# Kernel optimization log

Hardware: AMD Instinct MI355X
Metric: run time of the kernel (lower is better)

The kernel has to match this reference:

```python
import jax, jax.numpy as jnp
import numpy as np

B, T, S = 4, 2048, 512
HID, ND, NH = 2048, 1024, 16
HD = HID // NH  # 128
GATING_INIT = -4.0


def setup_inputs() -> dict:
    key = jax.random.key(0)
    ks = jax.random.split(key, 12)
    sc_h = 1.0 / np.sqrt(HID)
    sc_n = 1.0 / np.sqrt(ND)
    mask = jax.random.bernoulli(ks[2], 0.9, (B, S))
    mask = mask.at[:, 0].set(True)  # avoid fully-masked rows (NaN softmax)
    return {
        "hidden_states": jax.random.normal(ks[0], (B, T, HID), jnp.float32),
        "notes": jax.random.normal(ks[1], (B, S, ND), jnp.float32),
        "notes_mask": mask,
        "q_w": jax.random.normal(ks[3], (HID, HID), jnp.float32) * sc_h,
        "q_b": jax.random.normal(ks[4], (HID,), jnp.float32) * 0.01,
        "k_w": jax.random.normal(ks[5], (HID, ND), jnp.float32) * sc_n,
        "k_b": jax.random.normal(ks[6], (HID,), jnp.float32) * 0.01,
        "v_w": jax.random.normal(ks[7], (HID, ND), jnp.float32) * sc_n,
        "v_b": jax.random.normal(ks[8], (HID,), jnp.float32) * 0.01,
        "o_w": jax.random.normal(ks[9], (HID, HID), jnp.float32) * sc_h,
        "o_b": jax.random.normal(ks[10], (HID,), jnp.float32) * 0.01,
        "gate": jnp.full((1,), GATING_INIT, jnp.float32),
    }


def reference(hidden_states, notes, notes_mask, q_w, q_b, k_w, k_b, v_w, v_b, o_w, o_b, gate):
    # projections (torch Linear: x @ W^T + b)
    q = hidden_states @ q_w.T + q_b            # (B,T,HID)
    k = notes @ k_w.T + k_b                    # (B,S,HID)
    v = notes @ v_w.T + v_b                    # (B,S,HID)
    q = q.reshape(B, T, NH, HD).transpose(0, 2, 1, 3)  # (B,H,T,D)
    k = k.reshape(B, S, NH, HD).transpose(0, 2, 1, 3)  # (B,H,S,D)
    v = v.reshape(B, S, NH, HD).transpose(0, 2, 1, 3)
    scores = jnp.einsum("bhtd,bhsd->bhts", q, k) / jnp.sqrt(jnp.float32(HD))
    scores = jnp.where(notes_mask[:, None, None, :], scores, -jnp.inf)
    attn = jax.nn.softmax(scores, axis=-1)
    context = jnp.einsum("bhts,bhsd->bhtd", attn, v)   # (B,H,T,D)
    g = jax.nn.sigmoid(gate).reshape(1, 1, 1, 1)
    context = (g * context).transpose(0, 2, 1, 3).reshape(B, T, HID)
    delta = context @ o_w.T + o_b
    return delta
```

## Files before the change

kernel.cpp:

```cpp
#include <hip/hip_runtime.h>
#include <hip/hip_bf16.h>
#include <stdint.h>

#define B_ 4
#define T_ 2048
#define S_ 512
#define HID_ 2048
#define ND_ 1024
#define NH_ 16
#define HD_ 128

typedef unsigned short u16;
typedef unsigned int u32;
typedef __attribute__((ext_vector_type(8))) short bf16x8;
typedef __attribute__((ext_vector_type(4))) float f32x4;
typedef __attribute__((ext_vector_type(16))) float f32x16;
typedef __attribute__((ext_vector_type(4))) float f4;
typedef __attribute__((ext_vector_type(4))) u16 us4;
typedef __attribute__((ext_vector_type(8))) u16 us8;
typedef __attribute__((ext_vector_type(4))) u32 u32x4;

__device__ inline u16 f2bf(float f) {
  unsigned u = __builtin_bit_cast(unsigned, f);
  u += 0x7FFFu + ((u >> 16) & 1u);
  return (u16)(u >> 16);
}

__device__ inline u32 cvtpk(float lo, float hi) {
  u32 r;
  asm("v_cvt_pk_bf16_f32 %0, %1, %2" : "=v"(r) : "v"(lo), "v"(hi));
  return r;
}

__device__ inline f32x4 mfma16(bf16x8 a, bf16x8 b, f32x4 c) {
  return __builtin_amdgcn_mfma_f32_16x16x32_bf16(a, b, c, 0, 0, 0);
}
__device__ inline f32x16 mfma32(bf16x8 a, bf16x8 b, f32x16 c) {
  return __builtin_amdgcn_mfma_f32_32x32x16_bf16(a, b, c, 0, 0, 0);
}

__device__ inline void gload_lds16(const u16* g, u16* l) {
  __builtin_amdgcn_global_load_lds(
      (const __attribute__((address_space(1))) unsigned int*)g,
      (__attribute__((address_space(3))) unsigned int*)l, 16, 0, 0);
}

#define FENCED_BARRIER() asm volatile("s_barrier" ::: "memory")

__global__ __launch_bounds__(256) void convert_all(
    const float* __restrict__ h, const float* __restrict__ n,
    const float* __restrict__ qw, const float* __restrict__ kw,
    const float* __restrict__ vw, const float* __restrict__ ow,
    u16* __restrict__ dh, u16* __restrict__ dn, u16* __restrict__ dqw,
    u16* __restrict__ dkw, u16* __restrict__ dvw, u16* __restrict__ dow) {
  const int C0 = 4194304;
  const int C1 = C0 + 524288;
  const int C2 = C1 + 1048576;
  const int C3 = C2 + 524288;
  const int C4 = C3 + 524288;
  const int C5 = C4 + 1048576;
  for (int c = blockIdx.x * blockDim.x + threadIdx.x; c < C5;
       c += gridDim.x * blockDim.x) {
    const float* s; u16* d; int o;
    if (c < C0)      { s = h;  d = dh;  o = c; }
    else if (c < C1) { s = n;  d = dn;  o = c - C0; }
    else if (c < C2) { s = qw; d = dqw; o = c - C1; }
    else if (c < C3) { s = kw; d = dkw; o = c - C2; }
    else if (c < C4) { s = vw; d = dvw; o = c - C3; }
    else             { s = ow; d = dow; o = c - C4; }
    f4 v = ((const f4*)s)[o];
    us4 r = { f2bf(v[0]), f2bf(v[1]), f2bf(v[2]), f2bf(v[3]) };
    ((us4*)d)[o] = r;
  }
}

template <bool OUT_BF16>
__global__ __launch_bounds__(256) void gemm_bt(
    const u16* __restrict__ A, const u16* __restrict__ Bm,
    const float* __restrict__ bias, void* __restrict__ Cout,
    int M, int N, int K) {
  __shared__ u16 As[128 * 32];
  __shared__ u16 Bs[128 * 32];
  const int tid = threadIdx.x;
  const int lane = tid & 63;
  const int wave = tid >> 6;
  const int wr = (wave >> 1) * 64;
  const int wc = (wave & 1) * 64;
  const int c15 = lane & 15;
  const int g = lane >> 4;
  const int bx = blockIdx.x, by = blockIdx.y;

  const u16* gA = A + (size_t)(by * 128 + (tid >> 2)) * K + (tid & 3) * 8;
  const u16* gB = Bm + (size_t)(bx * 128 + (tid >> 2)) * K + (tid & 3) * 8;

  f32x4 acc[4][4];
#pragma unroll
  for (int i = 0; i < 4; ++i)
#pragma unroll
    for (int j = 0; j < 4; ++j) acc[i][j] = (f32x4){0.f, 0.f, 0.f, 0.f};

  for (int k0 = 0; k0 < K; k0 += 32) {
    gload_lds16(gA + k0, &As[wave * 512]);
    gload_lds16(gA + (size_t)64 * K + k0, &As[2048 + wave * 512]);
    gload_lds16(gB + k0, &Bs[wave * 512]);
    gload_lds16(gB + (size_t)64 * K + k0, &Bs[2048 + wave * 512]);
    __syncthreads();
    bf16x8 af[4], bfr[4];
#pragma unroll
    for (int mt = 0; mt < 4; ++mt)
      af[mt] = *(const bf16x8*)&As[(wr + mt * 16 + c15) * 32 + g * 8];
#pragma unroll
    for (int nt = 0; nt < 4; ++nt)
      bfr[nt] = *(const bf16x8*)&Bs[(wc + nt * 16 + c15) * 32 + g * 8];
#pragma unroll
    for (int mt = 0; mt < 4; ++mt)
#pragma unroll
      for (int nt = 0; nt < 4; ++nt)
        acc[mt][nt] = mfma16(af[mt], bfr[nt], acc[mt][nt]);
    __syncthreads();
  }

#pragma unroll
  for (int mt = 0; mt < 4; ++mt)
#pragma unroll
    for (int nt = 0; nt < 4; ++nt) {
      const int m = by * 128 + wr + mt * 16 + g * 4;
      const int n = bx * 128 + wc + nt * 16 + c15;
      const float bv = bias[n];
#pragma unroll
      for (int r = 0; r < 4; ++r) {
        const float v = acc[mt][nt][r] + bv;
        if (OUT_BF16)
          ((u16*)Cout)[(size_t)(m + r) * N + n] = f2bf(v);
        else
          ((float*)Cout)[(size_t)(m + r) * N + n] = v;
      }
    }
}

template <bool OUT_BF16>
__global__ __launch_bounds__(512, 2) void gemm_pipe(
    const u16* __restrict__ A, const u16* __restrict__ Bm,
    const float* __restrict__ bias, void* __restrict__ Cout,
    int M, int N, int K) {
  extern __shared__ u16 lds[];
  const int tid = threadIdx.x;
  const int lane = tid & 63, wave = tid >> 6;
  const int wm = wave >> 2, wn = wave & 3;
  const int c15 = lane & 15, g = lane >> 4;
  const int bid = blockIdx.y * gridDim.x + blockIdx.x;
  const int sw = (bid & 7) * 32 + (bid >> 3);
  const int bn = sw & 7, bm = sw >> 3;
  const int NT = K >> 5;

  const int srow = tid >> 2;
  const int sx = (tid & 3) ^ ((srow >> 1) & 3);
  const u16* pa0 = A + (size_t)(bm * 256 + srow) * K + sx * 8;
  const u16* pa1 = A + (size_t)(bm * 256 + 128 + srow) * K + sx * 8;
  const u16* pb0 = Bm + (size_t)(bn * 256 + srow) * K + sx * 8;
  const u16* pb1 = Bm + (size_t)(bn * 256 + 128 + srow) * K + sx * 8;

  const int xr = (c15 >> 1) & 3;
  const int aoff = wm * 4096 + c15 * 32 + (g ^ xr) * 8;
  const int boff = 8192 + wn * 2048 + c15 * 32 + (g ^ xr) * 8;

  f32x4 acc[8][4];
#pragma unroll
  for (int i = 0; i < 8; ++i)
#pragma unroll
    for (int j = 0; j < 4; ++j) acc[i][j] = (f32x4){0.f, 0.f, 0.f, 0.f};

  {
    u16* sA = lds + wave * 512;
    u16* sB = lds + 8192 + wave * 512;
    gload_lds16(pa0, sA);          gload_lds16(pa1, sA + 4096);
    gload_lds16(pb0, sB);          gload_lds16(pb1, sB + 4096);
    pa0 += 32; pa1 += 32; pb0 += 32; pb1 += 32;
    gload_lds16(pa0, sA + 16384);  gload_lds16(pa1, sA + 20480);
    gload_lds16(pb0, sB + 16384);  gload_lds16(pb1, sB + 20480);
    pa0 += 32; pa1 += 32; pb0 += 32; pb1 += 32;
  }
  asm volatile("s_waitcnt vmcnt(4)" ::: "memory");
  FENCED_BARRIER();

  for (int t = 0; t < NT; ++t) {
    const bool more = (t + 2 < NT);
    const u16* cb = lds + (t & 3) * 16384;
    u16* sb = lds + ((t + 2) & 3) * 16384;

    bf16x8 a[8], b[4];
#pragma unroll
    for (int mf = 0; mf < 4; ++mf)
      a[mf] = *(const bf16x8*)(cb + aoff + mf * 512);
#pragma unroll
    for (int nf = 0; nf < 4; ++nf)
      b[nf] = *(const bf16x8*)(cb + boff + nf * 512);
#pragma unroll
    for (int mf = 4; mf < 8; ++mf)
      a[mf] = *(const bf16x8*)(cb + aoff + mf * 512);

    if (more) {
      gload_lds16(pa0, sb + wave * 512);
      gload_lds16(pa1, sb + 4096 + wave * 512);
      gload_lds16(pb0, sb + 8192 + wave * 512);
      gload_lds16(pb1, sb + 12288 + wave * 512);
      pa0 += 32; pa1 += 32; pb0 += 32; pb1 += 32;
    }

    __builtin_amdgcn_s_setprio(1);
#pragma unroll
    for (int mf = 0; mf < 8; ++mf)
#pragma unroll
      for (int nf = 0; nf < 4; ++nf)
        acc[mf][nf] = mfma16(a[mf], b[nf], acc[mf][nf]);
    __builtin_amdgcn_s_setprio(0);

    if (more) asm volatile("s_waitcnt vmcnt(4)" ::: "memory");
    else      asm volatile("s_waitcnt vmcnt(0)" ::: "memory");
    FENCED_BARRIER();
  }

#pragma unroll
  for (int mf = 0; mf < 8; ++mf)
#pragma unroll
    for (int nf = 0; nf < 4; ++nf) {
      const int m = bm * 256 + wm * 128 + mf * 16 + g * 4;
      const int n = bn * 256 + wn * 64 + nf * 16 + c15;
      const float bv = bias[n];
#pragma unroll
      for (int r = 0; r < 4; ++r) {
        const float v = acc[mf][nf][r] + bv;
        if (OUT_BF16)
          ((u16*)Cout)[(size_t)(m + r) * N + n] = f2bf(v);
        else
          ((float*)Cout)[(size_t)(m + r) * N + n] = v;
      }
    }
}

__global__ __launch_bounds__(256) void transpose_v(const u16* __restrict__ v,
                                                   u16* __restrict__ vt) {
  __shared__ u16 tile[32][36];
  const int s0 = blockIdx.x * 32;
  const int bh = blockIdx.y;
  const int d0 = blockIdx.z * 32;
  const int b = bh >> 4, h = bh & 15;
  const int tid = threadIdx.x;
  const int sl = tid >> 3, dl = (tid & 7) * 4;
  us4 val = *(const us4*)(v + (size_t)(b * S_ + s0 + sl) * HID_ + h * HD_ + d0 + dl);
  *(us4*)&tile[sl][dl] = val;
  __syncthreads();
  const int dl2 = tid >> 3, sl2 = (tid & 7) * 4;
  us4 outv = { tile[sl2 + 0][dl2], tile[sl2 + 1][dl2],
               tile[sl2 + 2][dl2], tile[sl2 + 3][dl2] };
  *(us4*)(vt + ((size_t)bh * HD_ + d0 + dl2) * S_ + s0 + sl2) = outv;
}

__global__ __launch_bounds__(256) void attn_fwd(
    const u16* __restrict__ q, const u16* __restrict__ k,
    const u16* __restrict__ vt, const int* __restrict__ mask,
    const float* __restrict__ gate, u16* __restrict__ ctx) {
  __shared__ u16 smem[32768];
  __shared__ float addend[S_];
  const int tid = threadIdx.x, lane = tid & 63, wave = tid >> 6;
  const int bh = blockIdx.y, b = bh >> 4, h = bh & 15;
  const int tw = blockIdx.x * 128 + wave * 32;
  const int l31 = lane & 31, hi = lane >> 5;

  const u16* kb  = k + (size_t)b * S_ * HID_ + h * HD_;
  const u16* vtb = vt + (size_t)bh * HD_ * S_;

  const u16* sp[4];
  int dj[4];
  u16* ldsbase;
  ptrdiff_t stride;
  if (wave < 2) {
    ldsbase = smem;
    stride = 32 * HID_;
#pragma unroll
    for (int i = 0; i < 4; ++i) {
      const int jj = wave * 4 + i;
      const int row = jj * 4 + (lane >> 4);
      const int cb = (lane & 15) * 16;
      const int cbp = cb ^ ((row & 7) << 4);
      sp[i] = kb + (size_t)row * HID_ + (cbp >> 1);
      dj[i] = jj * 512;
    }
  } else {
    ldsbase = smem + 16384;
    stride = 32;
#pragma unroll
    for (int i = 0; i < 4; ++i) {
      const int jj = (wave - 2) * 4 + i;
      const int d = jj * 16 + (lane >> 2);
      const int cb = (lane & 3) * 16;
      const int cbp = cb ^ (((d >> 1) & 3) << 4);
      sp[i] = vtb + (size_t)d * S_ + (cbp >> 1);
      dj[i] = jj * 512;
    }
  }
#define STAGE(cur)                                            \
  do {                                                        \
    _Pragma("unroll") for (int i_ = 0; i_ < 4; ++i_) {        \
      gload_lds16(sp[i_], ldsbase + (cur) * 4096 + dj[i_]);   \
      sp[i_] += stride;                                       \
    }                                                         \
  } while (0)

  for (int s = tid; s < S_; s += 256)
    addend[s] = mask[b * S_ + s] ? 0.f : -1e30f;

  const u16* qrow = q + (size_t)(b * T_ + tw + l31) * HID_ + h * HD_;
  bf16x8 qf[8];
#pragma unroll
  for (int dc = 0; dc < 8; ++dc)
    qf[dc] = *(const bf16x8*)&qrow[dc * 16 + hi * 8];

  STAGE(0);
  STAGE(1);

  int kofs[8];
#pragma unroll
  for (int dc = 0; dc < 8; ++dc)
    kofs[dc] = l31 * 128 + (((dc * 32 + hi * 16) ^ ((l31 & 7) << 4)) >> 1);
  const int vswz = ((l31 >> 1) & 3) << 4;
  const int vcol0 = ((hi * 16) ^ vswz) >> 1;
  const int vcol1 = ((32 + hi * 16) ^ vswz) >> 1;

  float m_run = -1e30f, l_run = 0.f;
  f32x16 ct[4];
#pragma unroll
  for (int i = 0; i < 4; ++i)
#pragma unroll
    for (int r = 0; r < 16; ++r) ct[i][r] = 0.f;
  const float scale = 0.08838834764831845f;

  asm volatile("s_waitcnt vmcnt(4) lgkmcnt(0)" ::: "memory");
  FENCED_BARRIER();

  for (int it = 0; it < 16; ++it) {
    const int cur = it & 3;
    if (it + 2 < 16) STAGE((it + 2) & 3);
    const int s0 = it * 32;
    const u16* kt = smem + cur * 4096;
    const u16* vl = smem + 16384 + cur * 4096;

    f32x16 st_a, st_b;
#pragma unroll
    for (int r = 0; r < 16; ++r) { st_a[r] = 0.f; st_b[r] = 0.f; }
    __builtin_amdgcn_s_setprio(1);
#pragma unroll
    for (int dc = 0; dc < 4; ++dc) {
      bf16x8 kf0 = *(const bf16x8*)&kt[kofs[dc]];
      bf16x8 kf1 = *(const bf16x8*)&kt[kofs[4 + dc]];
      st_a = mfma32(kf0, qf[dc], st_a);
      st_b = mfma32(kf1, qf[4 + dc], st_b);
    }
    __builtin_amdgcn_s_setprio(0);

    float sc[16];
#pragma unroll
    for (int rq = 0; rq < 4; ++rq) {
      f4 ad = *(const f4*)&addend[s0 + rq * 8 + hi * 4];
#pragma unroll
      for (int m = 0; m < 4; ++m)
        sc[rq * 4 + m] = (st_a[rq * 4 + m] + st_b[rq * 4 + m]) * scale + ad[m];
    }
    float tm = sc[0];
#pragma unroll
    for (int i = 1; i < 16; ++i) tm = fmaxf(tm, sc[i]);
    tm = fmaxf(tm, __shfl_xor(tm, 32));
    const float nm = fmaxf(m_run, tm);
    if (!__all(nm - m_run <= 8.f)) {
      const float corr = __expf(m_run - nm);
      l_run *= corr;
#pragma unroll
      for (int db = 0; db < 4; ++db)
#pragma unroll
        for (int r = 0; r < 16; ++r) ct[db][r] *= corr;
      m_run = nm;
    }
    float p[16], ps = 0.f;
#pragma unroll
    for (int i = 0; i < 16; ++i) { p[i] = __expf(sc[i] - m_run); ps += p[i]; }
    ps += __shfl_xor(ps, 32);
    l_run += ps;

    u32 w[8], x[8];
#pragma unroll
    for (int q2 = 0; q2 < 4; ++q2) {
      w[2 * q2]     = cvtpk(p[4 * q2],     p[4 * q2 + 1]);
      w[2 * q2 + 1] = cvtpk(p[4 * q2 + 2], p[4 * q2 + 3]);
    }
#pragma unroll
    for (int i = 0; i < 8; ++i) x[i] = __shfl_xor((int)w[i], 32);
    const u32x4 f0 = hi ? (u32x4){x[2], x[3], w[2], w[3]}
                        : (u32x4){w[0], w[1], x[0], x[1]};
    const u32x4 f1 = hi ? (u32x4){x[6], x[7], w[6], w[7]}
                        : (u32x4){w[4], w[5], x[4], x[5]};
    const bf16x8 pf0 = __builtin_bit_cast(bf16x8, f0);
    const bf16x8 pf1 = __builtin_bit_cast(bf16x8, f1);

    __builtin_amdgcn_s_setprio(1);
#pragma unroll
    for (int db = 0; db < 4; ++db) {
      bf16x8 vf0 = *(const bf16x8*)&vl[db * 1024 + l31 * 32 + vcol0];
      ct[db] = mfma32(vf0, pf0, ct[db]);
      bf16x8 vf1 = *(const bf16x8*)&vl[db * 1024 + l31 * 32 + vcol1];
      ct[db] = mfma32(vf1, pf1, ct[db]);
    }
    __builtin_amdgcn_s_setprio(0);

    if (it < 15) {
      if (it < 14) asm volatile("s_waitcnt vmcnt(4)" ::: "memory");
      else         asm volatile("s_waitcnt vmcnt(0)" ::: "memory");
      FENCED_BARRIER();
    }
  }
#undef STAGE

  __syncthreads();

  const float gsig = 1.f / (1.f + __expf(-gate[0]));
  const float inv = gsig / l_run;
  u16* c_lds = smem + wave * 4352;
#pragma unroll
  for (int db = 0; db < 4; ++db)
#pragma unroll
    for (int rq = 0; rq < 4; ++rq) {
      us4 o = { f2bf(ct[db][rq * 4 + 0] * inv), f2bf(ct[db][rq * 4 + 1] * inv),
                f2bf(ct[db][rq * 4 + 2] * inv), f2bf(ct[db][rq * 4 + 3] * inv) };
      *(us4*)&c_lds[l31 * 136 + db * 32 + rq * 8 + hi * 4] = o;
    }
  u16* crow = ctx + (size_t)(b * T_ + tw) * HID_ + h * HD_;
#pragma unroll
  for (int rep = 0; rep < 8; ++rep) {
    const int tt = (lane >> 4) + rep * 4;
    us8 valv = *(const us8*)&c_lds[tt * 136 + (lane & 15) * 8];
    *(us8*)&crow[(size_t)tt * HID_ + (lane & 15) * 8] = valv;
  }
}

extern "C" void kernel_launch(void* const* d_in, const int* in_sizes, int n_in,
                              void* d_out, int out_size, void* d_ws, size_t ws_size,
                              hipStream_t stream) {
  (void)in_sizes; (void)n_in; (void)out_size; (void)ws_size;
  const float* hs   = (const float*)d_in[0];
  const float* nts  = (const float*)d_in[1];
  const int*   mask = (const int*)d_in[2];
  const float* qw   = (const float*)d_in[3];
  const float* qb   = (const float*)d_in[4];
  const float* kw   = (const float*)d_in[5];
  const float* kbi  = (const float*)d_in[6];
  const float* vw   = (const float*)d_in[7];
  const float* vbi  = (const float*)d_in[8];
  const float* ow   = (const float*)d_in[9];
  const float* obi  = (const float*)d_in[10];
  const float* gate = (const float*)d_in[11];
  float* out = (float*)d_out;

  char* w = (char*)d_ws;
  u16* h_bf   = (u16*)(w + 0);
  u16* n_bf   = (u16*)(w + 33554432);
  u16* qw_bf  = (u16*)(w + 37748736);
  u16* kw_bf  = (u16*)(w + 46137344);
  u16* vw_bf  = (u16*)(w + 50331648);
  u16* ow_bf  = (u16*)(w + 54525952);
  u16* q_bf   = (u16*)(w + 62914560);
  u16* k_bf   = (u16*)(w + 96468992);
  u16* v_bf   = (u16*)(w + 104857600);
  u16* vt_bf  = (u16*)(w + 113246208);
  u16* ctx_bf = h_bf;

  hipFuncSetAttribute(reinterpret_cast<const void*>(&gemm_pipe<true>),
                      hipFuncAttributeMaxDynamicSharedMemorySize, 131072);
  hipFuncSetAttribute(reinterpret_cast<const void*>(&gemm_pipe<false>),
                      hipFuncAttributeMaxDynamicSharedMemorySize, 131072);

  convert_all<<<dim3(2048), dim3(256), 0, stream>>>(
      hs, nts, qw, kw, vw, ow, h_bf, n_bf, qw_bf, kw_bf, vw_bf, ow_bf);
  gemm_bt<true><<<dim3(16, 16), dim3(256), 0, stream>>>(
      n_bf, kw_bf, kbi, k_bf, 2048, 2048, 1024);
  gemm_bt<true><<<dim3(16, 16), dim3(256), 0, stream>>>(
      n_bf, vw_bf, vbi, v_bf, 2048, 2048, 1024);
  transpose_v<<<dim3(16, 64, 4), dim3(256), 0, stream>>>(v_bf, vt_bf);
  gemm_pipe<true><<<dim3(8, 32), dim3(512), 131072, stream>>>(
      h_bf, qw_bf, qb, q_bf, 8192, 2048, 2048);
  attn_fwd<<<dim3(16, 64), dim3(256), 0, stream>>>(
      q_bf, k_bf, vt_bf, mask, gate, ctx_bf);
  gemm_pipe<false><<<dim3(8, 32), dim3(512), 131072, stream>>>(
      ctx_bf, ow_bf, obi, out, 8192, 2048, 2048);
}
```

Baseline: 282.5 us.

## Rewrite Q/O GEMM with 4 fat waves using 32x32 MFMA tiles

Replaces the 8-wave 256x256 GEMM built on 16x16x32 MFMAs with a 4-wave version where each wave owns a 128x128 output tile and issues 32x32x16 MFMAs. Each wave now reuses more data per LDS read and issues fewer, larger matrix instructions. In exchange it runs fewer waves per CU, which can hurt latency hiding, and uses 256 accumulator registers per wave. The output store pattern changes to match the 32x32 accumulator layout.

```diff
diff --git a/kernel.cpp b/kernel.cpp
--- a/kernel.cpp
+++ b/kernel.cpp
@@ -139,48 +139,57 @@
 }
 
 template <bool OUT_BF16>
-__global__ __launch_bounds__(512, 2) void gemm_pipe(
+__global__ __launch_bounds__(256, 1) void gemm_fat(
     const u16* __restrict__ A, const u16* __restrict__ Bm,
     const float* __restrict__ bias, void* __restrict__ Cout,
     int M, int N, int K) {
   extern __shared__ u16 lds[];
   const int tid = threadIdx.x;
   const int lane = tid & 63, wave = tid >> 6;
-  const int wm = wave >> 2, wn = wave & 3;
-  const int c15 = lane & 15, g = lane >> 4;
+  const int wm = wave >> 1, wn = wave & 1;
+  const int l31 = lane & 31, hi = lane >> 5;
   const int bid = blockIdx.y * gridDim.x + blockIdx.x;
   const int sw = (bid & 7) * 32 + (bid >> 3);
   const int bn = sw & 7, bm = sw >> 3;
   const int NT = K >> 5;
 
-  const int srow = tid >> 2;
-  const int sx = (tid & 3) ^ ((srow >> 1) & 3);
-  const u16* pa0 = A + (size_t)(bm * 256 + srow) * K + sx * 8;
-  const u16* pa1 = A + (size_t)(bm * 256 + 128 + srow) * K + sx * 8;
-  const u16* pb0 = Bm + (size_t)(bn * 256 + srow) * K + sx * 8;
-  const u16* pb1 = Bm + (size_t)(bn * 256 + 128 + srow) * K + sx * 8;
-
-  const int xr = (c15 >> 1) & 3;
-  const int aoff = wm * 4096 + c15 * 32 + (g ^ xr) * 8;
-  const int boff = 8192 + wn * 2048 + c15 * 32 + (g ^ xr) * 8;
-
-  f32x4 acc[8][4];
-#pragma unroll
-  for (int i = 0; i < 8; ++i)
-#pragma unroll
-    for (int j = 0; j < 4; ++j) acc[i][j] = (f32x4){0.f, 0.f, 0.f, 0.f};
-
-  {
-    u16* sA = lds + wave * 512;
-    u16* sB = lds + 8192 + wave * 512;
-    gload_lds16(pa0, sA);          gload_lds16(pa1, sA + 4096);
-    gload_lds16(pb0, sB);          gload_lds16(pb1, sB + 4096);
-    pa0 += 32; pa1 += 32; pb0 += 32; pb1 += 32;
-    gload_lds16(pa0, sA + 16384);  gload_lds16(pa1, sA + 20480);
-    gload_lds16(pb0, sB + 16384);  gload_lds16(pb1, sB + 20480);
-    pa0 += 32; pa1 += 32; pb0 += 32; pb1 += 32;
-  }
-  asm volatile("s_waitcnt vmcnt(4)" ::: "memory");
+  const u16* pA[4]; const u16* pB[4];
+  int dj[4];
+#pragma unroll
+  for (int i = 0; i < 4; ++i) {
+    const int c = (i * 4 + wave) * 64 + lane;
+    const int row = c >> 2;
+    const int sx = (c & 3) ^ ((row >> 1) & 3);
+    pA[i] = A + (size_t)(bm * 256 + row) * K + sx * 8;
+    pB[i] = Bm + (size_t)(bn * 256 + row) * K + sx * 8;
+    dj[i] = (i * 4 + wave) * 512;
+  }
+
+  const int swz3 = ((l31 >> 1) & 3) << 3;
+  const int aoff0 = (wm * 128 + l31) * 32 + ((hi * 8) ^ swz3);
+  const int aoff1 = aoff0 ^ 16;
+  const int boff0 = 8192 + (wn * 128 + l31) * 32 + ((hi * 8) ^ swz3);
+  const int boff1 = boff0 ^ 16;
+
+  f32x16 acc[4][4];
+#pragma unroll
+  for (int i = 0; i < 4; ++i)
+#pragma unroll
+    for (int j = 0; j < 4; ++j)
+#pragma unroll
+      for (int r = 0; r < 16; ++r) acc[i][j][r] = 0.f;
+
+#pragma unroll
+  for (int i = 0; i < 4; ++i) { gload_lds16(pA[i], lds + dj[i]);
+                                gload_lds16(pB[i], lds + 8192 + dj[i]); }
+#pragma unroll
+  for (int i = 0; i < 4; ++i) { pA[i] += 32; pB[i] += 32; }
+#pragma unroll
+  for (int i = 0; i < 4; ++i) { gload_lds16(pA[i], lds + 16384 + dj[i]);
+                                gload_lds16(pB[i], lds + 24576 + dj[i]); }
+#pragma unroll
+  for (int i = 0; i < 4; ++i) { pA[i] += 32; pB[i] += 32; }
+  asm volatile("s_waitcnt vmcnt(8)" ::: "memory");
   FENCED_BARRIER();
 
   for (int t = 0; t < NT; ++t) {
@@ -188,52 +197,56 @@
     const u16* cb = lds + (t & 3) * 16384;
     u16* sb = lds + ((t + 2) & 3) * 16384;
 
-    bf16x8 a[8], b[4];
-#pragma unroll
-    for (int mf = 0; mf < 4; ++mf)
-      a[mf] = *(const bf16x8*)(cb + aoff + mf * 512);
-#pragma unroll
-    for (int nf = 0; nf < 4; ++nf)
-      b[nf] = *(const bf16x8*)(cb + boff + nf * 512);
-#pragma unroll
-    for (int mf = 4; mf < 8; ++mf)
-      a[mf] = *(const bf16x8*)(cb + aoff + mf * 512);
+    bf16x8 a0[4], a1[4], b0[4], b1[4];
+#pragma unroll
+    for (int f = 0; f < 4; ++f) {
+      a0[f] = *(const bf16x8*)(cb + aoff0 + f * 1024);
+      a1[f] = *(const bf16x8*)(cb + aoff1 + f * 1024);
+      b0[f] = *(const bf16x8*)(cb + boff0 + f * 1024);
+      b1[f] = *(const bf16x8*)(cb + boff1 + f * 1024);
+    }
 
     if (more) {
-      gload_lds16(pa0, sb + wave * 512);
-      gload_lds16(pa1, sb + 4096 + wave * 512);
-      gload_lds16(pb0, sb + 8192 + wave * 512);
-      gload_lds16(pb1, sb + 12288 + wave * 512);
-      pa0 += 32; pa1 += 32; pb0 += 32; pb1 += 32;
+#pragma unroll
+      for (int i = 0; i < 4; ++i) { gload_lds16(pA[i], sb + dj[i]);
+                                    gload_lds16(pB[i], sb + 8192 + dj[i]); }
+#pragma unroll
+      for (int i = 0; i < 4; ++i) { pA[i] += 32; pB[i] += 32; }
     }
 
     __builtin_amdgcn_s_setprio(1);
 #pragma unroll
-    for (int mf = 0; mf < 8; ++mf)
-#pragma unroll
-      for (int nf = 0; nf < 4; ++nf)
-        acc[mf][nf] = mfma16(a[mf], b[nf], acc[mf][nf]);
+    for (int fa = 0; fa < 4; ++fa)
+#pragma unroll
+      for (int fb = 0; fb < 4; ++fb)
+        acc[fa][fb] = mfma32(a0[fa], b0[fb], acc[fa][fb]);
+#pragma unroll
+    for (int fa = 0; fa < 4; ++fa)
+#pragma unroll
+      for (int fb = 0; fb < 4; ++fb)
+        acc[fa][fb] = mfma32(a1[fa], b1[fb], acc[fa][fb]);
     __builtin_amdgcn_s_setprio(0);
 
-    if (more) asm volatile("s_waitcnt vmcnt(4)" ::: "memory");
+    if (more) asm volatile("s_waitcnt vmcnt(8)" ::: "memory");
     else      asm volatile("s_waitcnt vmcnt(0)" ::: "memory");
     FENCED_BARRIER();
   }
 
 #pragma unroll
-  for (int mf = 0; mf < 8; ++mf)
-#pragma unroll
-    for (int nf = 0; nf < 4; ++nf) {
-      const int m = bm * 256 + wm * 128 + mf * 16 + g * 4;
-      const int n = bn * 256 + wn * 64 + nf * 16 + c15;
+  for (int fa = 0; fa < 4; ++fa)
+#pragma unroll
+    for (int fb = 0; fb < 4; ++fb) {
+      const int n = bn * 256 + wn * 128 + fb * 32 + l31;
       const float bv = bias[n];
 #pragma unroll
-      for (int r = 0; r < 4; ++r) {
-        const float v = acc[mf][nf][r] + bv;
+      for (int r = 0; r < 16; ++r) {
+        const int m = bm * 256 + wm * 128 + fa * 32 +
+                      (r & 3) + 8 * (r >> 2) + 4 * hi;
+        const float v = acc[fa][fb][r] + bv;
         if (OUT_BF16)
-          ((u16*)Cout)[(size_t)(m + r) * N + n] = f2bf(v);
+          ((u16*)Cout)[(size_t)m * N + n] = f2bf(v);
         else
-          ((float*)Cout)[(size_t)(m + r) * N + n] = v;
+          ((float*)Cout)[(size_t)m * N + n] = v;
       }
     }
 }
@@ -472,9 +485,9 @@
   u16* vt_bf  = (u16*)(w + 113246208);
   u16* ctx_bf = h_bf;
 
-  hipFuncSetAttribute(reinterpret_cast<const void*>(&gemm_pipe<true>),
+  hipFuncSetAttribute(reinterpret_cast<const void*>(&gemm_fat<true>),
                       hipFuncAttributeMaxDynamicSharedMemorySize, 131072);
-  hipFuncSetAttribute(reinterpret_cast<const void*>(&gemm_pipe<false>),
+  hipFuncSetAttribute(reinterpret_cast<const void*>(&gemm_fat<false>),
                       hipFuncAttributeMaxDynamicSharedMemorySize, 131072);
 
   convert_all<<<dim3(2048), dim3(256), 0, stream>>>(
@@ -484,10 +497,10 @@
   gemm_bt<true><<<dim3(16, 16), dim3(256), 0, stream>>>(
       n_bf, vw_bf, vbi, v_bf, 2048, 2048, 1024);
   transpose_v<<<dim3(16, 64, 4), dim3(256), 0, stream>>>(v_bf, vt_bf);
-  gemm_pipe<true><<<dim3(8, 32), dim3(512), 131072, stream>>>(
+  gemm_fat<true><<<dim3(8, 32), dim3(256), 131072, stream>>>(
       h_bf, qw_bf, qb, q_bf, 8192, 2048, 2048);
   attn_fwd<<<dim3(16, 64), dim3(256), 0, stream>>>(
       q_bf, k_bf, vt_bf, mask, gate, ctx_bf);
-  gemm_pipe<false><<<dim3(8, 32), dim3(512), 131072, stream>>>(
+  gemm_fat<false><<<dim3(8, 32), dim3(256), 131072, stream>>>(
       ctx_bf, ow_bf, obi, out, 8192, 2048, 2048);
 }
```

New measurement: 296.4 us. 4.9% more time.
